# Optimization experiments

Hardware: AMD Instinct MI355X
Metric: run time of the kernel (lower is better)

Reference implementation:

```python
import jax, jax.numpy as jnp
import numpy as np

NUM_EXPERTS = 8
TOP_K = 2
D_MODEL = 1024
EXPERT_CAP = 512  # dim_feedforward // num_experts = 4096 // 8
B, S = 4, 2048


def setup_inputs() -> dict:
    key = jax.random.key(0)
    ks = jax.random.split(key, 4)
    scale = 1.0 / np.sqrt(D_MODEL)
    x = jax.random.normal(ks[0], (B, S, D_MODEL), dtype=jnp.float32)
    gate_w = jax.random.normal(ks[1], (D_MODEL, NUM_EXPERTS), dtype=jnp.float32) * scale
    w1 = jax.random.normal(ks[2], (NUM_EXPERTS, D_MODEL, EXPERT_CAP), dtype=jnp.float32) * scale
    b1 = jnp.zeros((NUM_EXPERTS, EXPERT_CAP), dtype=jnp.float32)
    w2 = jax.random.normal(ks[3], (NUM_EXPERTS, EXPERT_CAP, D_MODEL), dtype=jnp.float32) * (1.0 / np.sqrt(EXPERT_CAP))
    b2 = jnp.zeros((NUM_EXPERTS, D_MODEL), dtype=jnp.float32)
    return {"x": x, "gate_w": gate_w, "w1": w1, "b1": b1, "w2": w2, "b2": b2}


def reference(x, gate_w, w1, b1, w2, b2):
    Bx, Sx, D = x.shape
    xt = x.reshape(-1, D)  # [N, D], N = B*S
    gates = jax.nn.softmax(xt @ gate_w, axis=-1)           # [N, E]
    topk_g, topk_i = jax.lax.top_k(gates, TOP_K)           # [N, K]
    # Faithful to source: every selected expert is scaled by the SUM of all top-k gates
    tok_w = topk_g.sum(axis=-1)                            # [N]
    sel = (topk_i[:, :, None] == jnp.arange(NUM_EXPERTS)[None, None, :]).any(axis=1)  # [N, E] bool
    # Dense per-expert MLP (E small), then mask-combine (scatter-add equivalent)
    h = jax.nn.gelu(jnp.einsum('nd,edh->enh', xt, w1) + b1[:, None, :], approximate=False)  # [E, N, H]
    y = jnp.einsum('enh,ehd->end', h, w2) + b2[:, None, :]  # [E, N, D]
    out = jnp.einsum('end,ne,n->nd', y, sel.astype(x.dtype), tok_w)  # [N, D]
    return out.reshape(Bx, Sx, D)
```

## Files before the change

kernel.cpp:

```cpp
#include <hip/hip_runtime.h>
#include <math.h>

#define N_TOK 8192
#define DM 1024
#define NE 8
#define HE 512
#define NPAIR 16384

#define BM 128
#define BN 128
#define BK 64

#define GSTR 1028

typedef __bf16 bf16x8 __attribute__((ext_vector_type(8)));
typedef float f32x4 __attribute__((ext_vector_type(4)));

#define GLOBAL_AS __attribute__((address_space(1)))
#define LDS_AS    __attribute__((address_space(3)))

__device__ __forceinline__ void gl_lds16(const void* g, void* lds) {
    __builtin_amdgcn_global_load_lds((const GLOBAL_AS unsigned int*)g,
                                     (LDS_AS unsigned int*)lds, 16, 0, 0);
}

__device__ __forceinline__ unsigned short f2bf(float f) {
    unsigned int u = __float_as_uint(f);
    u += 0x7fffu + ((u >> 16) & 1u);
    return (unsigned short)(u >> 16);
}

__device__ __forceinline__ float bf2f(unsigned short u) {
    return __uint_as_float(((unsigned int)u) << 16);
}

__device__ __forceinline__ float gelu_exact(float v) {
    return 0.5f * v * (1.0f + erff(v * 0.70710678118654752440f));
}

__device__ __forceinline__ double shfl_xor_dbl(double v, int m) {
    long long l = __double_as_longlong(v);
    int lo = (int)(l & 0xffffffffll);
    int hi = (int)(l >> 32);
    lo = __shfl_xor(lo, m, 64);
    hi = __shfl_xor(hi, m, 64);
    return __longlong_as_double(((long long)hi << 32) | (unsigned long long)(unsigned int)lo);
}

__global__ void cast_x_kernel(const float* __restrict__ x, unsigned short* __restrict__ xb) {
    int i = blockIdx.x * 256 + threadIdx.x;
    float4 v = ((const float4*)x)[i];
    ushort4 o;
    o.x = f2bf(v.x); o.y = f2bf(v.y); o.z = f2bf(v.z); o.w = f2bf(v.w);
    ((ushort4*)xb)[i] = o;
}

__global__ void transpose_cast_kernel(const float* __restrict__ src,
                                      unsigned short* __restrict__ dst,
                                      int R, int C) {
    __shared__ float tile[64][65];
    const float* s = src + (size_t)blockIdx.z * R * C;
    unsigned short* d = dst + (size_t)blockIdx.z * R * C;
    int c0 = blockIdx.x * 64, r0 = blockIdx.y * 64;
    int tc = threadIdx.x & 63, tg = threadIdx.x >> 6;
    #pragma unroll
    for (int i = 0; i < 16; i++) {
        int r = tg * 16 + i;
        tile[r][tc] = s[(size_t)(r0 + r) * C + (c0 + tc)];
    }
    __syncthreads();
    #pragma unroll
    for (int i = 0; i < 16; i++) {
        int r = tg * 16 + i;
        d[(size_t)(c0 + r) * R + (r0 + tc)] = f2bf(tile[tc][r]);
    }
}

__global__ __launch_bounds__(256) void gate_kernel(
        const float* __restrict__ x, const float* __restrict__ gw,
        float* __restrict__ w_tok, int* __restrict__ e_sel) {
    __shared__ float gls[NE * GSTR];
    int tid = threadIdx.x;
    for (int v = tid; v < 2048; v += 256) {
        float4 g4 = ((const float4*)gw)[v];
        int idx = v * 4;
        int d = idx >> 3;
        int e0 = idx & 7;
        gls[(e0    ) * GSTR + d] = g4.x;
        gls[(e0 + 1) * GSTR + d] = g4.y;
        gls[(e0 + 2) * GSTR + d] = g4.z;
        gls[(e0 + 3) * GSTR + d] = g4.w;
    }
    __syncthreads();

    int n = blockIdx.x * 4 + (tid >> 6);
    int lane = tid & 63;
    const float4* xr = (const float4*)(x + (size_t)n * DM);

    double s[NE];
    #pragma unroll
    for (int e = 0; e < NE; e++) s[e] = 0.0;

    #pragma unroll
    for (int i = 0; i < 4; i++) {
        float4 x4 = xr[i * 64 + lane];
        int d = (i * 64 + lane) * 4;
        #pragma unroll
        for (int e = 0; e < NE; e++) {
            float4 g4 = *(const float4*)(&gls[e * GSTR + d]);
            s[e] += (double)x4.x * (double)g4.x + (double)x4.y * (double)g4.y
                  + (double)x4.z * (double)g4.z + (double)x4.w * (double)g4.w;
        }
    }
    #pragma unroll
    for (int e = 0; e < NE; e++) {
        for (int off = 32; off > 0; off >>= 1)
            s[e] += shfl_xor_dbl(s[e], off);
    }
    if (lane == 0) {
        double m = s[0];
        for (int e = 1; e < NE; e++) if (s[e] > m) m = s[e];
        double sum = 0.0;
        for (int e = 0; e < NE; e++) sum += exp(s[e] - m);
        int i1 = 0; double v1 = s[0];
        for (int e = 1; e < NE; e++) if (s[e] > v1) { v1 = s[e]; i1 = e; }
        int i2 = -1; double v2 = -1e300;
        for (int e = 0; e < NE; e++) if (e != i1 && s[e] > v2) { v2 = s[e]; i2 = e; }
        w_tok[n] = (float)((exp(v1 - m) + exp(v2 - m)) / sum);
        e_sel[2 * n]     = i1;
        e_sel[2 * n + 1] = i2;
    }
}

__global__ __launch_bounds__(1024) void route_kernel(
        const int* __restrict__ e_sel, int* __restrict__ cnt, int* __restrict__ offs,
        int* __restrict__ pair_tok, int* __restrict__ slotmap) {
    __shared__ int wbin[16][NE];
    __shared__ int wstart[16][NE];
    int tid = threadIdx.x;
    int w = tid >> 6, l = tid & 63;
    if (l < NE) wbin[w][l] = 0;
    __syncthreads();

    int sel[16];
    #pragma unroll
    for (int k = 0; k < 16; k++) {
        sel[k] = e_sel[tid * 16 + k];
        atomicAdd(&wbin[w][sel[k]], 1);
    }
    __syncthreads();

    if (tid == 0) {
        int a = 0;
        for (int e = 0; e < NE; e++) {
            int t = 0;
            for (int ww = 0; ww < 16; ww++) t += wbin[ww][e];
            cnt[e] = t; offs[e] = a;
            int r = a;
            for (int ww = 0; ww < 16; ww++) { wstart[ww][e] = r; r += wbin[ww][e]; }
            a += t;
        }
    }
    __syncthreads();
    if (l < NE) wbin[w][l] = wstart[w][l];
    __syncthreads();

    #pragma unroll
    for (int k = 0; k < 16; k++) {
        int i = tid * 16 + k;
        int slot = atomicAdd(&wbin[w][sel[k]], 1);
        pair_tok[slot] = i >> 1;
        slotmap[i] = slot;
    }
}

__global__ __launch_bounds__(256, 2) void gemm1_kernel(
        const unsigned short* __restrict__ xb,
        const unsigned short* __restrict__ w1t,
        const float* __restrict__ b1,
        const int* __restrict__ pair_tok,
        const int* __restrict__ cnt, const int* __restrict__ offs,
        unsigned short* __restrict__ hbuf) {
    int e = blockIdx.z;
    int cn = cnt[e];
    int m0 = blockIdx.y * BM;
    if (m0 >= cn) return;
    int n0 = blockIdx.x * BN;
    int base = offs[e];

    __shared__ __align__(16) unsigned short As[BM * BK];
    __shared__ __align__(16) unsigned short Bs[BN * BK];
    __shared__ int tks[BM];

    int tid = threadIdx.x;
    if (tid < BM) {
        int r = m0 + tid;
        tks[tid] = pair_tok[base + (r < cn ? r : 0)];
    }
    __syncthreads();

    int lane = tid & 63;
    int w = tid >> 6;
    int wu = __builtin_amdgcn_readfirstlane(w);
    int l3 = lane >> 3, l7 = lane & 7;
    int g = l7 ^ l3;

    const char* aptr[4];
    const char* bptr[4];
    #pragma unroll
    for (int j = 0; j < 4; j++) {
        int row = w * 32 + j * 8 + l3;
        aptr[j] = (const char*)xb  + (size_t)tks[row] * (DM * 2) + g * 16;
        bptr[j] = (const char*)w1t + ((size_t)e * HE + n0 + row) * (DM * 2) + g * 16;
    }

    int wm = (w & 1) * 64;
    int wn = (w >> 1) * 64;
    int fr = lane & 15;
    int fq = lane >> 4;

    f32x4 acc[4][4];
    #pragma unroll
    for (int i = 0; i < 4; i++)
        #pragma unroll
        for (int j = 0; j < 4; j++)
            acc[i][j] = (f32x4){0.f, 0.f, 0.f, 0.f};

    for (int k0 = 0; k0 < DM; k0 += BK) {
        int kb = k0 * 2;
        #pragma unroll
        for (int j = 0; j < 4; j++) {
            gl_lds16(aptr[j] + kb, (char*)As + wu * 4096 + j * 1024);
            gl_lds16(bptr[j] + kb, (char*)Bs + wu * 4096 + j * 1024);
        }
        __syncthreads();
        #pragma unroll
        for (int kk2 = 0; kk2 < 2; kk2++) {
            int sw = ((kk2 * 4 + fq) ^ (fr & 7)) << 4;
            bf16x8 af[4], bfv[4];
            #pragma unroll
            for (int i = 0; i < 4; i++)
                af[i] = *(const bf16x8*)((const char*)As + (wm + i * 16 + fr) * 128 + sw);
            #pragma unroll
            for (int j = 0; j < 4; j++)
                bfv[j] = *(const bf16x8*)((const char*)Bs + (wn + j * 16 + fr) * 128 + sw);
            #pragma unroll
            for (int i = 0; i < 4; i++)
                #pragma unroll
                for (int j = 0; j < 4; j++)
                    acc[i][j] = __builtin_amdgcn_mfma_f32_16x16x32_bf16(af[i], bfv[j], acc[i][j], 0, 0, 0);
        }
        __syncthreads();
    }

    #pragma unroll
    for (int j = 0; j < 4; j++) {
        int nn = n0 + wn + j * 16 + fr;
        float bias = b1[e * HE + nn];
        #pragma unroll
        for (int i = 0; i < 4; i++) {
            #pragma unroll
            for (int r = 0; r < 4; r++) {
                int mm = wm + i * 16 + fq * 4 + r;
                if (m0 + mm < cn) {
                    float v = acc[i][j][r] + bias;
                    hbuf[(size_t)(base + m0 + mm) * HE + nn] = f2bf(gelu_exact(v));
                }
            }
        }
    }
}

__global__ __launch_bounds__(256, 2) void gemm2_kernel(
        const unsigned short* __restrict__ hbuf,
        const unsigned short* __restrict__ w2t,
        const float* __restrict__ b2,
        const int* __restrict__ pair_tok,
        const float* __restrict__ w_tok,
        const int* __restrict__ cnt, const int* __restrict__ offs,
        unsigned short* __restrict__ ybuf) {
    int e = blockIdx.z;
    int cn = cnt[e];
    int m0 = blockIdx.y * BM;
    if (m0 >= cn) return;
    int n0 = blockIdx.x * BN;
    int base = offs[e];

    __shared__ __align__(16) unsigned short As[BM * BK];
    __shared__ __align__(16) unsigned short Bs[BN * BK];
    __shared__ float wts[BM];

    int tid = threadIdx.x;
    if (tid < BM) {
        int r = m0 + tid;
        int rr = (r < cn ? r : cn - 1);
        wts[tid] = w_tok[pair_tok[base + rr]];
    }
    __syncthreads();

    int lane = tid & 63;
    int w = tid >> 6;
    int wu = __builtin_amdgcn_readfirstlane(w);
    int l3 = lane >> 3, l7 = lane & 7;
    int g = l7 ^ l3;

    const char* aptr[4];
    const char* bptr[4];
    #pragma unroll
    for (int j = 0; j < 4; j++) {
        int row = w * 32 + j * 8 + l3;
        int crow = (m0 + row < cn) ? row : 0;
        aptr[j] = (const char*)hbuf + (size_t)(base + m0 + crow) * (HE * 2) + g * 16;
        bptr[j] = (const char*)w2t  + ((size_t)e * DM + n0 + row) * (HE * 2) + g * 16;
    }

    int wm = (w & 1) * 64;
    int wn = (w >> 1) * 64;
    int fr = lane & 15;
    int fq = lane >> 4;

    f32x4 acc[4][4];
    #pragma unroll
    for (int i = 0; i < 4; i++)
        #pragma unroll
        for (int j = 0; j < 4; j++)
            acc[i][j] = (f32x4){0.f, 0.f, 0.f, 0.f};

    for (int k0 = 0; k0 < HE; k0 += BK) {
        int kb = k0 * 2;
        #pragma unroll
        for (int j = 0; j < 4; j++) {
            gl_lds16(aptr[j] + kb, (char*)As + wu * 4096 + j * 1024);
            gl_lds16(bptr[j] + kb, (char*)Bs + wu * 4096 + j * 1024);
        }
        __syncthreads();
        #pragma unroll
        for (int kk2 = 0; kk2 < 2; kk2++) {
            int sw = ((kk2 * 4 + fq) ^ (fr & 7)) << 4;
            bf16x8 af[4], bfv[4];
            #pragma unroll
            for (int i = 0; i < 4; i++)
                af[i] = *(const bf16x8*)((const char*)As + (wm + i * 16 + fr) * 128 + sw);
            #pragma unroll
            for (int j = 0; j < 4; j++)
                bfv[j] = *(const bf16x8*)((const char*)Bs + (wn + j * 16 + fr) * 128 + sw);
            #pragma unroll
            for (int i = 0; i < 4; i++)
                #pragma unroll
                for (int j = 0; j < 4; j++)
                    acc[i][j] = __builtin_amdgcn_mfma_f32_16x16x32_bf16(af[i], bfv[j], acc[i][j], 0, 0, 0);
        }
        __syncthreads();
    }

    #pragma unroll
    for (int j = 0; j < 4; j++) {
        int dd = n0 + wn + j * 16 + fr;
        float bias = b2[e * DM + dd];
        #pragma unroll
        for (int i = 0; i < 4; i++) {
            #pragma unroll
            for (int r = 0; r < 4; r++) {
                int mm = wm + i * 16 + fq * 4 + r;
                if (m0 + mm < cn) {
                    float wgt = wts[mm];
                    ybuf[(size_t)(base + m0 + mm) * DM + dd] = f2bf(wgt * (acc[i][j][r] + bias));
                }
            }
        }
    }
}

__global__ void combine_kernel(const unsigned short* __restrict__ yb,
                               const int* __restrict__ slotmap,
                               float* __restrict__ out) {
    int i = blockIdx.x * 256 + threadIdx.x;
    int n = i >> 8;
    int c = (i & 255) * 4;
    int s1 = slotmap[2 * n];
    int s2 = slotmap[2 * n + 1];
    ushort4 a = *(const ushort4*)(&yb[(size_t)s1 * DM + c]);
    ushort4 b = *(const ushort4*)(&yb[(size_t)s2 * DM + c]);
    float4 o;
    o.x = bf2f(a.x) + bf2f(b.x);
    o.y = bf2f(a.y) + bf2f(b.y);
    o.z = bf2f(a.z) + bf2f(b.z);
    o.w = bf2f(a.w) + bf2f(b.w);
    ((float4*)out)[i] = o;
}

extern "C" void kernel_launch(void* const* d_in, const int* in_sizes, int n_in,
                              void* d_out, int out_size, void* d_ws, size_t ws_size,
                              hipStream_t stream) {
    const float* x  = (const float*)d_in[0];
    const float* gw = (const float*)d_in[1];
    const float* w1 = (const float*)d_in[2];
    const float* b1 = (const float*)d_in[3];
    const float* w2 = (const float*)d_in[4];
    const float* b2 = (const float*)d_in[5];
    float* out = (float*)d_out;

    char* ws = (char*)d_ws;
    unsigned short* ybuf = (unsigned short*)(ws);
    unsigned short* xb   = (unsigned short*)(ws);
    unsigned short* w1t  = (unsigned short*)(ws + 16777216);
    unsigned short* w2t  = (unsigned short*)(ws + 33554432);
    unsigned short* hbuf = (unsigned short*)(ws + 41943040);
    float* w_tok         = (float*)(ws + 58720256);
    int*   e_sel         = (int*)(ws + 58753024);
    int*   slotmap       = (int*)(ws + 58818560);
    int*   cnt           = (int*)(ws + 58884096);
    int*   offs          = (int*)(ws + 58884128);
    int*   pair_tok      = (int*)(ws + 58884224);

    cast_x_kernel<<<8192, 256, 0, stream>>>(x, xb);
    transpose_cast_kernel<<<dim3(HE / 64, DM / 64, NE), 256, 0, stream>>>(w1, w1t, DM, HE);
    transpose_cast_kernel<<<dim3(DM / 64, HE / 64, NE), 256, 0, stream>>>(w2, w2t, HE, DM);
    gate_kernel<<<N_TOK / 4, 256, 0, stream>>>(x, gw, w_tok, e_sel);
    route_kernel<<<1, 1024, 0, stream>>>(e_sel, cnt, offs, pair_tok, slotmap);
    gemm1_kernel<<<dim3(HE / BN, N_TOK / BM, NE), 256, 0, stream>>>(
        xb, w1t, b1, pair_tok, cnt, offs, hbuf);
    gemm2_kernel<<<dim3(DM / BN, N_TOK / BM, NE), 256, 0, stream>>>(
        hbuf, w2t, b2, pair_tok, w_tok, cnt, offs, ybuf);
    combine_kernel<<<(N_TOK * DM / 4) / 256, 256, 0, stream>>>(ybuf, slotmap, out);
}
```

Baseline: 262.0 us.

## Fuse cast kernels, double-buffer gemm1 LDS, parallelize route scan, raise gemm2 occupancy

```diff
diff --git a/kernel.cpp b/kernel.cpp
--- a/kernel.cpp
+++ b/kernel.cpp
@@ -47,37 +47,38 @@
     return __longlong_as_double(((long long)hi << 32) | (unsigned long long)(unsigned int)lo);
 }
 
-__global__ void cast_x_kernel(const float* __restrict__ x, unsigned short* __restrict__ xb) {
-    int i = blockIdx.x * 256 + threadIdx.x;
-    float4 v = ((const float4*)x)[i];
-    ushort4 o;
-    o.x = f2bf(v.x); o.y = f2bf(v.y); o.z = f2bf(v.z); o.w = f2bf(v.w);
-    ((ushort4*)xb)[i] = o;
-}
-
-__global__ void transpose_cast_kernel(const float* __restrict__ src,
-                                      unsigned short* __restrict__ dst,
-                                      int R, int C) {
+__global__ void transpose_cast2_kernel(const float* __restrict__ w1,
+                                       const float* __restrict__ w2,
+                                       unsigned short* __restrict__ w1t,
+                                       unsigned short* __restrict__ w2t) {
     __shared__ float tile[64][65];
-    const float* s = src + (size_t)blockIdx.z * R * C;
-    unsigned short* d = dst + (size_t)blockIdx.z * R * C;
-    int c0 = blockIdx.x * 64, r0 = blockIdx.y * 64;
+    int z = blockIdx.z;
+    const float* src; unsigned short* dst; int R, C, c0, r0;
+    if (z < 8) {
+        src = w1 + (size_t)z * DM * HE; dst = w1t + (size_t)z * DM * HE;
+        R = DM; C = HE; c0 = blockIdx.x * 64; r0 = blockIdx.y * 64;
+    } else {
+        int e = z - 8;
+        src = w2 + (size_t)e * HE * DM; dst = w2t + (size_t)e * HE * DM;
+        R = HE; C = DM; c0 = blockIdx.y * 64; r0 = blockIdx.x * 64;
+    }
     int tc = threadIdx.x & 63, tg = threadIdx.x >> 6;
     #pragma unroll
     for (int i = 0; i < 16; i++) {
         int r = tg * 16 + i;
-        tile[r][tc] = s[(size_t)(r0 + r) * C + (c0 + tc)];
+        tile[r][tc] = src[(size_t)(r0 + r) * C + (c0 + tc)];
     }
     __syncthreads();
     #pragma unroll
     for (int i = 0; i < 16; i++) {
         int r = tg * 16 + i;
-        d[(size_t)(c0 + r) * R + (r0 + tc)] = f2bf(tile[tc][r]);
-    }
-}
-
-__global__ __launch_bounds__(256) void gate_kernel(
+        dst[(size_t)(c0 + r) * R + (r0 + tc)] = f2bf(tile[tc][r]);
+    }
+}
+
+__global__ __launch_bounds__(256) void gate_cast_kernel(
         const float* __restrict__ x, const float* __restrict__ gw,
+        unsigned short* __restrict__ xb,
         float* __restrict__ w_tok, int* __restrict__ e_sel) {
     __shared__ float gls[NE * GSTR];
     int tid = threadIdx.x;
@@ -96,6 +97,7 @@
     int n = blockIdx.x * 4 + (tid >> 6);
     int lane = tid & 63;
     const float4* xr = (const float4*)(x + (size_t)n * DM);
+    ushort4* xw = (ushort4*)(xb + (size_t)n * DM);
 
     double s[NE];
     #pragma unroll
@@ -104,6 +106,9 @@
     #pragma unroll
     for (int i = 0; i < 4; i++) {
         float4 x4 = xr[i * 64 + lane];
+        ushort4 o;
+        o.x = f2bf(x4.x); o.y = f2bf(x4.y); o.z = f2bf(x4.z); o.w = f2bf(x4.w);
+        xw[i * 64 + lane] = o;
         int d = (i * 64 + lane) * 4;
         #pragma unroll
         for (int e = 0; e < NE; e++) {
@@ -137,6 +142,7 @@
         int* __restrict__ pair_tok, int* __restrict__ slotmap) {
     __shared__ int wbin[16][NE];
     __shared__ int wstart[16][NE];
+    __shared__ int etot[NE], eoffs[NE];
     int tid = threadIdx.x;
     int w = tid >> 6, l = tid & 63;
     if (l < NE) wbin[w][l] = 0;
@@ -150,16 +156,22 @@
     }
     __syncthreads();
 
+    if (tid < NE) {
+        int t = 0;
+        for (int ww = 0; ww < 16; ww++) t += wbin[ww][tid];
+        etot[tid] = t;
+    }
+    __syncthreads();
     if (tid == 0) {
         int a = 0;
-        for (int e = 0; e < NE; e++) {
-            int t = 0;
-            for (int ww = 0; ww < 16; ww++) t += wbin[ww][e];
-            cnt[e] = t; offs[e] = a;
-            int r = a;
-            for (int ww = 0; ww < 16; ww++) { wstart[ww][e] = r; r += wbin[ww][e]; }
-            a += t;
-        }
+        for (int e = 0; e < NE; e++) { eoffs[e] = a; a += etot[e]; }
+    }
+    __syncthreads();
+    if (tid < NE) {
+        cnt[tid] = etot[tid];
+        offs[tid] = eoffs[tid];
+        int r = eoffs[tid];
+        for (int ww = 0; ww < 16; ww++) { wstart[ww][tid] = r; r += wbin[ww][tid]; }
     }
     __syncthreads();
     if (l < NE) wbin[w][l] = wstart[w][l];
@@ -188,17 +200,10 @@
     int n0 = blockIdx.x * BN;
     int base = offs[e];
 
-    __shared__ __align__(16) unsigned short As[BM * BK];
-    __shared__ __align__(16) unsigned short Bs[BN * BK];
-    __shared__ int tks[BM];
+    __shared__ __align__(16) unsigned short As[2 * BM * BK];
+    __shared__ __align__(16) unsigned short Bs[2 * BN * BK];
 
     int tid = threadIdx.x;
-    if (tid < BM) {
-        int r = m0 + tid;
-        tks[tid] = pair_tok[base + (r < cn ? r : 0)];
-    }
-    __syncthreads();
-
     int lane = tid & 63;
     int w = tid >> 6;
     int wu = __builtin_amdgcn_readfirstlane(w);
@@ -210,7 +215,9 @@
     #pragma unroll
     for (int j = 0; j < 4; j++) {
         int row = w * 32 + j * 8 + l3;
-        aptr[j] = (const char*)xb  + (size_t)tks[row] * (DM * 2) + g * 16;
+        int r = m0 + row;
+        int t = pair_tok[base + (r < cn ? r : 0)];
+        aptr[j] = (const char*)xb  + (size_t)t * (DM * 2) + g * 16;
         bptr[j] = (const char*)w1t + ((size_t)e * HE + n0 + row) * (DM * 2) + g * 16;
     }
 
@@ -226,31 +233,45 @@
         for (int j = 0; j < 4; j++)
             acc[i][j] = (f32x4){0.f, 0.f, 0.f, 0.f};
 
-    for (int k0 = 0; k0 < DM; k0 += BK) {
-        int kb = k0 * 2;
-        #pragma unroll
-        for (int j = 0; j < 4; j++) {
-            gl_lds16(aptr[j] + kb, (char*)As + wu * 4096 + j * 1024);
-            gl_lds16(bptr[j] + kb, (char*)Bs + wu * 4096 + j * 1024);
-        }
-        __syncthreads();
+    #pragma unroll
+    for (int j = 0; j < 4; j++) {
+        gl_lds16(aptr[j], (char*)As + wu * 4096 + j * 1024);
+        gl_lds16(bptr[j], (char*)Bs + wu * 4096 + j * 1024);
+    }
+
+    for (int it = 0; it < DM / BK; it++) {
+        int p = it & 1;
+        if (it + 1 < DM / BK) {
+            int kb = (it + 1) * (BK * 2);
+            #pragma unroll
+            for (int j = 0; j < 4; j++) {
+                gl_lds16(aptr[j] + kb, (char*)As + (p ^ 1) * 16384 + wu * 4096 + j * 1024);
+                gl_lds16(bptr[j] + kb, (char*)Bs + (p ^ 1) * 16384 + wu * 4096 + j * 1024);
+            }
+            asm volatile("s_waitcnt vmcnt(8)" ::: "memory");
+        } else {
+            asm volatile("s_waitcnt vmcnt(0)" ::: "memory");
+        }
+        __builtin_amdgcn_s_barrier();
+        const char* ab = (const char*)As + p * 16384;
+        const char* bb = (const char*)Bs + p * 16384;
         #pragma unroll
         for (int kk2 = 0; kk2 < 2; kk2++) {
             int sw = ((kk2 * 4 + fq) ^ (fr & 7)) << 4;
             bf16x8 af[4], bfv[4];
             #pragma unroll
             for (int i = 0; i < 4; i++)
-                af[i] = *(const bf16x8*)((const char*)As + (wm + i * 16 + fr) * 128 + sw);
+                af[i] = *(const bf16x8*)(ab + (wm + i * 16 + fr) * 128 + sw);
             #pragma unroll
             for (int j = 0; j < 4; j++)
-                bfv[j] = *(const bf16x8*)((const char*)Bs + (wn + j * 16 + fr) * 128 + sw);
+                bfv[j] = *(const bf16x8*)(bb + (wn + j * 16 + fr) * 128 + sw);
             #pragma unroll
             for (int i = 0; i < 4; i++)
                 #pragma unroll
                 for (int j = 0; j < 4; j++)
                     acc[i][j] = __builtin_amdgcn_mfma_f32_16x16x32_bf16(af[i], bfv[j], acc[i][j], 0, 0, 0);
         }
-        __syncthreads();
+        __builtin_amdgcn_s_barrier();
     }
 
     #pragma unroll
@@ -271,7 +292,7 @@
     }
 }
 
-__global__ __launch_bounds__(256, 2) void gemm2_kernel(
+__global__ __launch_bounds__(256, 4) void gemm2_kernel(
         const unsigned short* __restrict__ hbuf,
         const unsigned short* __restrict__ w2t,
         const float* __restrict__ b2,
@@ -413,10 +434,8 @@
     int*   offs          = (int*)(ws + 58884128);
     int*   pair_tok      = (int*)(ws + 58884224);
 
-    cast_x_kernel<<<8192, 256, 0, stream>>>(x, xb);
-    transpose_cast_kernel<<<dim3(HE / 64, DM / 64, NE), 256, 0, stream>>>(w1, w1t, DM, HE);
-    transpose_cast_kernel<<<dim3(DM / 64, HE / 64, NE), 256, 0, stream>>>(w2, w2t, HE, DM);
-    gate_kernel<<<N_TOK / 4, 256, 0, stream>>>(x, gw, w_tok, e_sel);
+    transpose_cast2_kernel<<<dim3(8, 16, 16), 256, 0, stream>>>(w1, w2, w1t, w2t);
+    gate_cast_kernel<<<N_TOK / 4, 256, 0, stream>>>(x, gw, xb, w_tok, e_sel);
     route_kernel<<<1, 1024, 0, stream>>>(e_sel, cnt, offs, pair_tok, slotmap);
     gemm1_kernel<<<dim3(HE / BN, N_TOK / BM, NE), 256, 0, stream>>>(
         xb, w1t, b1, pair_tok, cnt, offs, hbuf);
```

New measurement: 260.0 us. No clear change (-0.8%).
